# Performance work log

Hardware: AMD Instinct MI355X
Metric: run time of the kernel (lower is better)

## Reference

```python
import jax, jax.numpy as jnp
import numpy as np

B, NUM, NVAR = 2048, 100, 11
NUM_OBS, NC = 10, 3
T_FIN = 10.0
RHO_OBS = 1.0; RHO_INEQ = 1.0; RHO_LANE = 1.0; RHO_PROJ = 1.0
W_SMOOTH = 20.0; W_VDES = 2.0; W_YDES = 1.0
A_EGO = 3.0; B_EGO = 1.5; MARGIN = 0.2
V_MIN = 0.001; V_MAX = 18.0; A_MAX = 6.0
MAXITER = 5
H = 256

def _basis():
    s = np.linspace(0.0, 1.0, NUM)
    j = np.arange(NVAR)
    P = s[:, None] ** j[None, :]
    Pd = np.zeros((NUM, NVAR)); Pdd = np.zeros((NUM, NVAR))
    Pd[:, 1:] = j[1:][None, :] * s[:, None] ** (j[1:] - 1)[None, :]
    Pdd[:, 2:] = (j[2:] * (j[2:] - 1))[None, :] * s[:, None] ** (j[2:] - 2)[None, :]
    return (jnp.asarray(P, jnp.float32), jnp.asarray(Pd / T_FIN, jnp.float32),
            jnp.asarray(Pdd / (T_FIN ** 2), jnp.float32))

P, PDOT, PDDOT = _basis()
A_EQ_X = jnp.stack([P[0], PDOT[0], PDDOT[0], P[-1]])   # [4, NVAR]
A_EQ_Y = jnp.stack([P[0], PDOT[0], PDDOT[0]])          # [3, NVAR]
PTP = P.T @ P

def _kkt_inv(Q, A):
    m = A.shape[0]
    K = jnp.concatenate([jnp.concatenate([Q, A.T], axis=1),
                         jnp.concatenate([A, jnp.zeros((m, m), jnp.float32)], axis=1)], axis=0)
    return jnp.linalg.inv(K)

# ADMM cost: rho_proj*I + smoothness + rho_obs*A_obs^T A_obs + rho_ineq*(Pdot^T Pdot + Pddot^T Pddot)
Q_COMMON = (RHO_PROJ + W_SMOOTH) * jnp.eye(NVAR, dtype=jnp.float32) \
    + RHO_OBS * NUM_OBS * NC * PTP \
    + RHO_INEQ * (PDOT.T @ PDOT + PDDOT.T @ PDDOT)
KKT_X = _kkt_inv(Q_COMMON, A_EQ_X)
KKT_Y = _kkt_inv(Q_COMMON + 2.0 * RHO_LANE * PTP, A_EQ_Y)   # A_lane = [P; -P]
# x_init QP (smoothness + v_des / y_des tracking)
Q_IX = W_SMOOTH * jnp.eye(NVAR, dtype=jnp.float32) + W_VDES * (PDOT.T @ PDOT)
KKT_IX = _kkt_inv(Q_IX, A_EQ_X)
KKT_IY = _kkt_inv(Q_IX + W_YDES * PTP, A_EQ_Y)


def _forward(init_state_ego, goal_des, closest_obs, psi_obs, dim_x_obs, dim_y_obs,
             y_ub, y_lb, gru_W_ih, gru_W_hh, gru_b, gru_h0,
             mlp_W1, mlp_b1, mlp_W2, mlp_b2):
    b = init_state_ego.shape[0]
    x0, y0, vx0, vy0, ax0, ay0 = (init_state_ego[:, i] for i in range(6))
    b_eq_x = jnp.stack([x0, vx0, ax0, goal_des[:, 0]], axis=1)   # [B,4]
    b_eq_y = jnp.stack([y0, vy0, ay0], axis=1)                    # [B,3]

    # ---- obstacle circle trajectories (static obstacles, vx=vy=0) ----
    xo = closest_obs[:, :NUM_OBS]; yo = closest_obs[:, NUM_OBS:2 * NUM_OBS]   # [B,O]
    r = jnp.stack([jnp.zeros_like(dim_x_obs),
                   (dim_x_obs - dim_y_obs) / 2,
                   -(dim_x_obs - dim_y_obs) / 2], axis=2)                      # [B,O,3]
    x_circ = xo[:, :, None] + r * jnp.cos(psi_obs)[:, :, None]                # [B,O,3]
    y_circ = yo[:, :, None] + r * jnp.sin(psi_obs)[:, :, None]
    shape4 = (b, NUM_OBS, NC, NUM)
    x_obs_f = jnp.broadcast_to(x_circ[..., None], shape4).reshape(b, -1)      # [B,O*C*T]
    y_obs_f = jnp.broadcast_to(y_circ[..., None], shape4).reshape(b, -1)
    rad = dim_y_obs / 2
    a_obs = jnp.broadcast_to((A_EGO + rad + MARGIN)[:, :, None, None], shape4).reshape(b, -1)
    b_obs = jnp.broadcast_to((B_EGO + rad + MARGIN)[:, :, None, None], shape4).reshape(b, -1)

    # ---- GRU context over obstacles -> learned lambda init ----
    feats = jnp.stack([xo, yo, dim_x_obs, dim_y_obs, psi_obs], axis=2)        # [B,O,5]
    def gru_step(h, x):
        gx = x @ gru_W_ih + gru_b
        gh = h @ gru_W_hh
        z = jax.nn.sigmoid(gx[:, :H] + gh[:, :H])
        rg = jax.nn.sigmoid(gx[:, H:2 * H] + gh[:, H:2 * H])
        n = jnp.tanh(gx[:, 2 * H:] + rg * gh[:, 2 * H:])
        return (1.0 - z) * n + z * h, None
    hT, _ = jax.lax.scan(gru_step, jnp.broadcast_to(gru_h0, (b, H)), jnp.swapaxes(feats, 0, 1))
    lam = jax.nn.relu(hT @ mlp_W1 + mlp_b1) @ mlp_W2 + mlp_b2                 # [B,2*NVAR]
    lam_x, lam_y = lam[:, :NVAR], lam[:, NVAR:]

    # ---- x_init: equality-constrained smoothness/tracking QP ----
    v_des = jnp.sqrt(vx0 ** 2 + vy0 ** 2)
    lin_ix = W_VDES * v_des[:, None] * jnp.sum(PDOT, axis=0)[None, :]
    lin_iy = W_YDES * goal_des[:, 1:2] * jnp.sum(P, axis=0)[None, :]
    c_x0 = (jnp.concatenate([lin_ix, b_eq_x], 1) @ KKT_IX.T)[:, :NVAR]
    c_y0 = (jnp.concatenate([lin_iy, b_eq_y], 1) @ KKT_IY.T)[:, :NVAR]

    b_lane = jnp.concatenate([y_ub[:, None] * jnp.ones((1, NUM), jnp.float32),
                              -y_lb[:, None] * jnp.ones((1, NUM), jnp.float32)], axis=1)  # [B,2T]

    def AobsT(v):   # A_obs^T v, v: [B, O*C*T] -> [B, NVAR]
        return v.reshape(b, NUM_OBS * NC, NUM).sum(axis=1) @ P

    def step(carry, _):
        c_x, c_y, lx, ly = carry
        x = c_x @ P.T; xd = c_x @ PDOT.T; xdd = c_x @ PDDOT.T
        y = c_y @ P.T; yd = c_y @ PDOT.T; ydd = c_y @ PDDOT.T
        wc = jnp.tile(x, (1, NUM_OBS * NC)) - x_obs_f
        ws = jnp.tile(y, (1, NUM_OBS * NC)) - y_obs_f
        alpha_o = jnp.arctan2(ws * a_obs, wc * b_obs)
        ca, sa = jnp.cos(alpha_o), jnp.sin(alpha_o)
        c1 = RHO_OBS * (a_obs ** 2 * ca ** 2 + b_obs ** 2 * sa ** 2)
        c2 = RHO_OBS * (a_obs * wc * ca + b_obs * ws * sa)
        d_o = jnp.maximum(1.0, c2 / c1)
        alpha_v = jnp.clip(jnp.arctan2(yd, xd), -0.41, 0.41)
        cv, sv = jnp.cos(alpha_v), jnp.sin(alpha_v)
        d_v = jnp.clip(xd * cv + yd * sv, V_MIN, V_MAX)
        alpha_a = jnp.arctan2(ydd + 1e-4, xdd + 1e-4)
        caa, saa = jnp.cos(alpha_a), jnp.sin(alpha_a)
        d_a = jnp.clip(xdd * caa + ydd * saa, 0.0, A_MAX)
        # targets
        b_ox = x_obs_f + a_obs * d_o * ca; b_oy = y_obs_f + b_obs * d_o * sa
        b_vx = d_v * cv; b_vy = d_v * sv
        b_ax = d_a * caa; b_ay = d_a * saa
        b_lane_aug = jnp.minimum(jnp.concatenate([y, -y], 1), b_lane)  # slack-augmented
        top_x = lx + RHO_PROJ * c_x0 + RHO_OBS * AobsT(b_ox) + RHO_INEQ * (b_vx @ PDOT + b_ax @ PDDOT)
        top_y = ly + RHO_PROJ * c_y0 + RHO_OBS * AobsT(b_oy) + RHO_INEQ * (b_vy @ PDOT + b_ay @ PDDOT) \
            + RHO_LANE * ((b_lane_aug[:, :NUM] - b_lane_aug[:, NUM:]) @ P)
        c_xn = (jnp.concatenate([top_x, b_eq_x], 1) @ KKT_X.T)[:, :NVAR]
        c_yn = (jnp.concatenate([top_y, b_eq_y], 1) @ KKT_Y.T)[:, :NVAR]
        # residuals / Lagrange multiplier updates
        xn = c_xn @ P.T; yn = c_yn @ P.T
        res_ox = jnp.tile(xn, (1, NUM_OBS * NC)) - b_ox
        res_oy = jnp.tile(yn, (1, NUM_OBS * NC)) - b_oy
        lxn = lx - RHO_OBS * AobsT(res_ox) \
            - RHO_INEQ * ((c_xn @ PDOT.T - b_vx) @ PDOT + (c_xn @ PDDOT.T - b_ax) @ PDDOT)
        res_lane = jnp.concatenate([yn, -yn], 1) - b_lane_aug
        lyn = ly - RHO_OBS * AobsT(res_oy) \
            - RHO_INEQ * ((c_yn @ PDOT.T - b_vy) @ PDOT + (c_yn @ PDDOT.T - b_ay) @ PDDOT) \
            - RHO_LANE * ((res_lane[:, :NUM] - res_lane[:, NUM:]) @ P)
        return (c_xn, c_yn, lxn, lyn), None

    (c_x, c_y, lam_x, lam_y), _ = jax.lax.scan(step, (c_x0, c_y0, lam_x, lam_y),
                                               None, length=MAXITER)
    return jnp.concatenate([c_x, c_y], axis=1)   # [B, 2*NVAR]


def setup_inputs() -> dict:
    key = jax.random.key(0)
    ks = jax.random.split(key, 12)
    d = {
        'init_state_ego': jax.random.normal(ks[0], (B, 6), jnp.float32),
        'goal_des': jax.random.normal(ks[1], (B, 2), jnp.float32),
        'closest_obs': jax.random.normal(ks[2], (B, 2 * NUM_OBS), jnp.float32),
        'psi_obs': jax.random.normal(ks[3], (B, NUM_OBS), jnp.float32),
        'dim_x_obs': jax.random.uniform(ks[4], (B, NUM_OBS), jnp.float32),
        'dim_y_obs': jax.random.uniform(ks[5], (B, NUM_OBS), jnp.float32),
        'y_ub': jnp.ones((B,), jnp.float32),
        'y_lb': jnp.zeros((B,), jnp.float32),
        'gru_W_ih': jax.random.normal(ks[6], (5, 3 * H), jnp.float32) / np.sqrt(5.0),
        'gru_W_hh': jax.random.normal(ks[7], (H, 3 * H), jnp.float32) / np.sqrt(float(H)),
        'gru_b': jnp.zeros((3 * H,), jnp.float32),
        'gru_h0': jax.random.normal(ks[8], (H,), jnp.float32) * 0.1,
        'mlp_W1': jax.random.normal(ks[9], (H, 512), jnp.float32) / np.sqrt(float(H)),
        'mlp_b1': jnp.zeros((512,), jnp.float32),
        'mlp_W2': jax.random.normal(ks[10], (512, 2 * NVAR), jnp.float32) / np.sqrt(512.0),
        'mlp_b2': jnp.zeros((2 * NVAR,), jnp.float32),
    }
    return d


def reference(init_state_ego, goal_des, closest_obs, psi_obs, dim_x_obs, dim_y_obs,
              y_ub, y_lb, gru_W_ih, gru_W_hh, gru_b, gru_h0,
              mlp_W1, mlp_b1, mlp_W2, mlp_b2):
    return _forward(init_state_ego, goal_des, closest_obs, psi_obs, dim_x_obs, dim_y_obs,
                    y_ub, y_lb, gru_W_ih, gru_W_hh, gru_b, gru_h0,
                    mlp_W1, mlp_b1, mlp_W2, mlp_b2)
```

## Files before the change

### kernel.cpp

```cpp
#include <hip/hip_runtime.h>
#include <math.h>

typedef short bf16x8 __attribute__((ext_vector_type(8)));
typedef float f32x4 __attribute__((ext_vector_type(4)));

__device__ __forceinline__ unsigned short f2bf(float x) {
  union { float f; unsigned u; } v; v.f = x;
  unsigned r = v.u + 0x7FFFu + ((v.u >> 16) & 1u);
  return (unsigned short)(r >> 16);
}
__device__ __forceinline__ float bf2f(unsigned short h) {
  union { unsigned u; float f; } v; v.u = ((unsigned)h) << 16; return v.f;
}

#define WS_WAUG  0u
#define WS_W1T   442368u
#define WS_HAUGA 704512u
#define WS_HAUGB 1884160u
#define WS_HF32  3063808u
#define WS_LAM   5160960u
#define WS_KKT   5341184u
#define WS_GX    5344000u
#define WS_GY    5344704u
#define WS_MX    5345408u
#define WS_MY    5346112u
#define WS_SUMS  5346816u
#define WS_W2T   5346944u

__global__ __launch_bounds__(256) void prep(
    const float* __restrict__ Whh, const float* __restrict__ Wih,
    const float* __restrict__ gb, const float* __restrict__ W1,
    const float* __restrict__ W2, const float* __restrict__ h0,
    const float* __restrict__ obs, const float* __restrict__ dimx,
    const float* __restrict__ dimy, const float* __restrict__ psi,
    unsigned short* __restrict__ Waug, unsigned short* __restrict__ W1T,
    unsigned short* __restrict__ W2T,
    unsigned short* __restrict__ HaugA, unsigned short* __restrict__ HaugB,
    float* __restrict__ kkt_out, float* __restrict__ Gx_out,
    float* __restrict__ Gy_out, float* __restrict__ Mx_out,
    float* __restrict__ My_out, float* __restrict__ sums_out)
{
  __shared__ double S[21];
  __shared__ double aug[15][32];
  __shared__ double fbuf[15];
  __shared__ double Md[11][11];
  if (blockIdx.x < 4) {
    const int mat = blockIdx.x;
    const int n = (mat == 0 || mat == 2) ? 15 : 14;
    const int twoN = 2 * n;
    if (threadIdx.x == 0) {
      for (int m = 0; m < 21; ++m) S[m] = 0.0;
      for (int s = 0; s < 100; ++s) {
        double t = s * (1.0 / 99.0);
        double p = 1.0;
        for (int m = 0; m < 21; ++m) { S[m] += p; p *= t; }
      }
    }
    __syncthreads();
    for (int idx = threadIdx.x; idx < n * twoN; idx += 256) {
      int r = idx / twoN, c = idx % twoN;
      double v;
      if (c >= n) v = (c - n == r) ? 1.0 : 0.0;
      else if (r < 11 && c < 11) {
        double ptp = S[r + c];
        double pdp = (r >= 1 && c >= 1) ? ((double)(r * c) / 100.0) * S[r + c - 2] : 0.0;
        double pddp = (r >= 2 && c >= 2) ? ((double)(r*(r-1)) * (double)(c*(c-1)) / 10000.0) * S[r + c - 4] : 0.0;
        double dg = (r == c) ? 1.0 : 0.0;
        if (mat == 0)      v = 21.0*dg + 30.0*ptp + pdp + pddp;
        else if (mat == 1) v = 21.0*dg + 32.0*ptp + pdp + pddp;
        else if (mat == 2) v = 20.0*dg + 2.0*pdp;
        else               v = 20.0*dg + 2.0*pdp + ptp;
      } else if (r >= 11 && c >= 11) v = 0.0;
      else {
        int ar = (r >= 11) ? (r - 11) : (c - 11);
        int ac = (r >= 11) ? c : r;
        v = (ar == 0) ? ((ac == 0) ? 1.0 : 0.0)
          : (ar == 1) ? ((ac == 1) ? 0.1 : 0.0)
          : (ar == 2) ? ((ac == 2) ? 0.02 : 0.0)
          : 1.0;
      }
      aug[r][c] = v;
    }
    __syncthreads();
    for (int p = 0; p < n; ++p) {
      double pv = aug[p][p];
      __syncthreads();
      double inv = 1.0 / pv;
      for (int c = threadIdx.x; c < twoN; c += 256) aug[p][c] *= inv;
      __syncthreads();
      if (threadIdx.x < n) fbuf[threadIdx.x] = aug[threadIdx.x][p];
      __syncthreads();
      for (int idx = threadIdx.x; idx < n * twoN; idx += 256) {
        int r = idx / twoN, c = idx % twoN;
        if (r != p) aug[r][c] -= fbuf[r] * aug[p][c];
      }
      __syncthreads();
    }
    for (int idx = threadIdx.x; idx < 11 * n; idx += 256) {
      int r = idx / n, c = idx % n;
      kkt_out[mat * 176 + r * 16 + c] = (float)aug[r][n + c];
    }
    if (mat < 2) {
      if (threadIdx.x < 121) {
        int j = threadIdx.x / 11, i = threadIdx.x % 11;
        double m = 30.0 * S[j + i];
        if (j >= 1 && i >= 1) m += ((double)(j * i) / 100.0) * S[j + i - 2];
        if (j >= 2 && i >= 2) m += ((double)(j*(j-1)) * (double)(i*(i-1)) / 10000.0) * S[j + i - 4];
        if (mat == 1) m += 2.0 * S[j + i];
        Md[j][i] = m;
      }
      __syncthreads();
      if (threadIdx.x < 121) {
        int j = threadIdx.x / 11, i = threadIdx.x % 11;
        double g = (j == i) ? 1.0 : 0.0;
        for (int k = 0; k < 11; ++k) g -= Md[j][k] * aug[k][n + i];
        if (mat == 0) { Gx_out[j * 16 + i] = (float)g; Mx_out[j * 16 + i] = (float)Md[j][i]; }
        else          { Gy_out[j * 16 + i] = (float)g; My_out[j * 16 + i] = (float)Md[j][i]; }
      }
    }
    if (mat == 0 && threadIdx.x < 11) {
      int j = threadIdx.x;
      sums_out[j] = (float)S[j];
      sums_out[11 + j] = (j >= 1) ? (float)((double)j / 10.0 * S[j - 1]) : 0.f;
    }
    return;
  }
  int idx = (blockIdx.x - 4) * 256 + threadIdx.x;
  if (idx < 221184) {
    int col = idx / 288, k = idx - col * 288;
    float v;
    if (k < 256)       v = Whh[k * 768 + col];
    else if (k < 261)  v = Wih[(k - 256) * 768 + col];
    else if (k == 261) v = gb[col];
    else               v = 0.f;
    Waug[idx] = f2bf(v);
  } else if (idx < 352256) {
    int j = idx - 221184;
    int col = j >> 8, k = j & 255;
    W1T[j] = f2bf(W1[k * 512 + col]);
  } else if (idx < 942080) {
    int j = idx - 352256;
    int row = j / 288, k = j - row * 288;
    float v;
    if (k < 256)       v = h0[k];
    else if (k == 256) v = obs[row * 20 + 0];
    else if (k == 257) v = obs[row * 20 + 10];
    else if (k == 258) v = dimx[row * 10 + 0];
    else if (k == 259) v = dimy[row * 10 + 0];
    else if (k == 260) v = psi[row * 10 + 0];
    else if (k == 261) v = 1.0f;
    else               v = 0.f;
    HaugA[row * 288 + k] = f2bf(v);
  } else if (idx < 995328) {
    int j = idx - 942080;
    int row = j / 26, k = 262 + (j - row * 26);
    HaugB[row * 288 + k] = 0;
  } else if (idx < 1011712) {
    int j = idx - 995328;
    int col = j >> 9, k = j & 511;
    W2T[j] = f2bf(col < 22 ? W2[k * 22 + col] : 0.f);
  }
}

#define MFMA __builtin_amdgcn_mfma_f32_16x16x32_bf16
__global__ __launch_bounds__(256) void gru_step(
    const unsigned short* __restrict__ Waug,
    const unsigned short* __restrict__ HaugC, unsigned short* __restrict__ HaugN,
    float* __restrict__ Hf32, const float* __restrict__ h0,
    const float* __restrict__ obs, const float* __restrict__ dimx,
    const float* __restrict__ dimy, const float* __restrict__ psi,
    int s)
{
  const int tid = threadIdx.x;
  const int m0 = blockIdx.x * 32;
  const int c0 = blockIdx.y * 32;
  const int lane = tid & 63, w = tid >> 6;
  const int l15 = lane & 15, g4 = lane >> 4;
  const int mi = w >> 1, cg = w & 1;

  const unsigned short* Arow = HaugC + (size_t)(m0 + mi * 16 + l15) * 288 + g4 * 8;
  const unsigned short* Bcol = Waug + (size_t)(c0 + cg * 16 + l15) * 288 + g4 * 8;

  f32x4 accz = {0.f,0.f,0.f,0.f}, accr = {0.f,0.f,0.f,0.f};
  f32x4 anh = {0.f,0.f,0.f,0.f}, anx = {0.f,0.f,0.f,0.f};

  #pragma unroll
  for (int kc = 0; kc < 9; ++kc) {
    bf16x8 a  = *(const bf16x8*)(Arow + kc * 32);
    bf16x8 bz = *(const bf16x8*)(Bcol + kc * 32);
    bf16x8 br = *(const bf16x8*)(Bcol + 256 * 288 + kc * 32);
    bf16x8 bn = *(const bf16x8*)(Bcol + 512 * 288 + kc * 32);
    accz = MFMA(a, bz, accz, 0, 0, 0);
    accr = MFMA(a, br, accr, 0, 0, 0);
    if (kc < 8) anh = MFMA(a, bn, anh, 0, 0, 0);
    else        anx = MFMA(a, bn, anx, 0, 0, 0);
  }

  const int colh = c0 + cg * 16 + l15;
  float h0c = (s == 0) ? h0[colh] : 0.f;
  #pragma unroll
  for (int rg = 0; rg < 4; ++rg) {
    int row = m0 + mi * 16 + g4 * 4 + rg;
    float hold = (s == 0) ? h0c : Hf32[(size_t)row * 256 + colh];
    float z = 1.f / (1.f + __expf(-accz[rg]));
    float rr = 1.f / (1.f + __expf(-accr[rg]));
    float nn = tanhf(anx[rg] + rr * anh[rg]);
    float hnew = (1.f - z) * nn + z * hold;
    Hf32[(size_t)row * 256 + colh] = hnew;
    HaugN[(size_t)row * 288 + colh] = f2bf(hnew);
  }
  if (blockIdx.y == 0 && s < 9 && tid < 192) {
    int row = m0 + tid / 6, e = tid - (tid / 6) * 6;
    int s1 = s + 1;
    float v = (e == 0) ? obs[row * 20 + s1] : (e == 1) ? obs[row * 20 + 10 + s1]
            : (e == 2) ? dimx[row * 10 + s1] : (e == 3) ? dimy[row * 10 + s1]
            : (e == 4) ? psi[row * 10 + s1] : 1.0f;
    HaugN[(size_t)row * 288 + 256 + e] = f2bf(v);
  }
}

__global__ __launch_bounds__(256) void mlp_fused(
    const unsigned short* __restrict__ Haug, const unsigned short* __restrict__ W1T,
    const float* __restrict__ b1, const unsigned short* __restrict__ W2T,
    const float* __restrict__ b2, float* __restrict__ lam)
{
  __shared__ __align__(16) unsigned short As[4096];
  __shared__ __align__(16) unsigned short Acts[8192];
  const int tid = threadIdx.x;
  const int m0 = blockIdx.x * 16;
  const int lane = tid & 63, w = tid >> 6, l15 = lane & 15, g4 = lane >> 4;

  #pragma unroll
  for (int r = 0; r < 2; ++r) {
    int j = tid + 256 * r;
    int tile = j >> 6, q = j & 63, ci = q >> 2, ks = q & 3;
    const unsigned short* src = Haug + (size_t)(m0 + ci) * 288 + tile * 32 + ks * 8;
    *(int4*)&As[tile * 512 + q * 8] = *(const int4*)src;
  }
  __syncthreads();
  const int foff = (l15 * 4 + g4) * 8;

  f32x4 acc[8];
  #pragma unroll
  for (int nt = 0; nt < 8; ++nt) acc[nt] = (f32x4){0.f,0.f,0.f,0.f};
  #pragma unroll
  for (int kc = 0; kc < 8; ++kc) {
    bf16x8 a = *(const bf16x8*)&As[kc * 512 + foff];
    int kk = kc * 32 + g4 * 8;
    #pragma unroll
    for (int nt = 0; nt < 8; ++nt) {
      int col = w * 128 + nt * 16 + l15;
      bf16x8 b = *(const bf16x8*)&W1T[(size_t)col * 256 + kk];
      acc[nt] = MFMA(a, b, acc[nt], 0, 0, 0);
    }
  }
  #pragma unroll
  for (int nt = 0; nt < 8; ++nt) {
    int col = w * 128 + nt * 16 + l15;
    float bb = b1[col];
    int tile = col >> 5, sub = (col >> 3) & 3, e = col & 7;
    #pragma unroll
    for (int rg = 0; rg < 4; ++rg) {
      int row = g4 * 4 + rg;
      float v = fmaxf(acc[nt][rg] + bb, 0.f);
      Acts[tile * 512 + (row * 4 + sub) * 8 + e] = f2bf(v);
    }
  }
  __syncthreads();

  if (w < 2) {
    int col = w * 16 + l15;
    f32x4 a2 = {0.f,0.f,0.f,0.f};
    #pragma unroll
    for (int kc = 0; kc < 16; ++kc) {
      bf16x8 a = *(const bf16x8*)&Acts[kc * 512 + foff];
      bf16x8 b = *(const bf16x8*)&W2T[(size_t)col * 512 + kc * 32 + g4 * 8];
      a2 = MFMA(a, b, a2, 0, 0, 0);
    }
    if (col < 22) {
      float bb = b2[col];
      #pragma unroll
      for (int rg = 0; rg < 4; ++rg)
        lam[(size_t)(m0 + g4 * 4 + rg) * 22 + col] = a2[rg] + bb;
    }
  }
}

__global__ __launch_bounds__(128) void solver(
    const float* __restrict__ ise, const float* __restrict__ goal,
    const float* __restrict__ obs, const float* __restrict__ psi,
    const float* __restrict__ dimx, const float* __restrict__ dimy,
    const float* __restrict__ yub, const float* __restrict__ ylb,
    const float* __restrict__ lam, const float* __restrict__ kkt,
    const float* __restrict__ Gxm, const float* __restrict__ Gym,
    const float* __restrict__ Mxm, const float* __restrict__ Mym,
    const float* __restrict__ sums, float* __restrict__ out)
{
  __shared__ __align__(16) float Pt[3][11][108];
  __shared__ __align__(16) float red[7][108];
  __shared__ float redout[7][11];
  __shared__ float cx[11], cy[11], lx[11], ly[11], cx0[11], cy0[11];
  __shared__ float kxB[11], kyB[11], hx[11], hy[11];
  __shared__ float rhsx[15], rhsy[14];
  __shared__ float xc[30], yc[30], sa_[10], sb_[10], sab[10], sab2[10];

  const int b = blockIdx.x;
  const int tid = threadIdx.x;

  if (tid < 100) {
    float t = tid * (1.0f / 99.0f);
    float tjm2 = 0.f, tjm1 = 0.f, tj = 1.f;
    #pragma unroll
    for (int j = 0; j < 11; ++j) {
      Pt[0][j][tid] = tj;
      Pt[1][j][tid] = 0.1f * (float)j * tjm1;
      Pt[2][j][tid] = 0.01f * (float)(j * (j - 1)) * tjm2;
      tjm2 = tjm1; tjm1 = tj; tj *= t;
    }
  }
  if (tid < 10) {
    int o = tid;
    float xo = obs[b * 20 + o], yo = obs[b * 20 + 10 + o];
    float dx = dimx[b * 10 + o], dy = dimy[b * 10 + o], ps = psi[b * 10 + o];
    float sp, cp;
    __sincosf(ps, &sp, &cp);
    float r1 = 0.5f * (dx - dy);
    xc[o * 3] = xo; xc[o * 3 + 1] = xo + r1 * cp; xc[o * 3 + 2] = xo - r1 * cp;
    yc[o * 3] = yo; yc[o * 3 + 1] = yo + r1 * sp; yc[o * 3 + 2] = yo - r1 * sp;
    float rad = 0.5f * dy;
    float av = 3.2f + rad, bv = 1.7f + rad;
    sa_[o] = av; sb_[o] = bv; sab[o] = av * bv; sab2[o] = av * bv * av * bv;
  }
  if (tid < 11) { lx[tid] = lam[b * 22 + tid]; ly[tid] = lam[b * 22 + 11 + tid]; }
  const float vx0 = ise[b * 6 + 2], vy0 = ise[b * 6 + 3];
  if (tid == 0) {
    float x0 = ise[b * 6 + 0], y0 = ise[b * 6 + 1];
    float ax0 = ise[b * 6 + 4], ay0 = ise[b * 6 + 5];
    rhsx[11] = x0; rhsx[12] = vx0; rhsx[13] = ax0; rhsx[14] = goal[b * 2 + 0];
    rhsy[11] = y0; rhsy[12] = vy0; rhsy[13] = ay0;
  }
  {
    float vdes = sqrtf(vx0 * vx0 + vy0 * vy0);
    float gy = goal[b * 2 + 1];
    if (tid < 11) { rhsx[tid] = 2.f * vdes * sums[11 + tid]; rhsy[tid] = gy * sums[tid]; }
  }
  const float yU = yub[b], yL = ylb[b];
  __syncthreads();
  if (tid < 11) {
    const float* K = kkt + 2 * 176 + tid * 16;
    float s = 0.f;
    #pragma unroll
    for (int j = 0; j < 15; ++j) s += K[j] * rhsx[j];
    cx0[tid] = s; cx[tid] = s;
    const float* Kx = kkt + tid * 16;
    float kb = 0.f;
    #pragma unroll
    for (int c = 0; c < 4; ++c) kb += Kx[11 + c] * rhsx[11 + c];
    kxB[tid] = kb;
  } else if (tid >= 16 && tid < 27) {
    int i = tid - 16;
    const float* K = kkt + 3 * 176 + i * 16;
    float s = 0.f;
    #pragma unroll
    for (int j = 0; j < 14; ++j) s += K[j] * rhsy[j];
    cy0[i] = s; cy[i] = s;
    const float* Ky = kkt + 176 + i * 16;
    float kb = 0.f;
    #pragma unroll
    for (int c = 0; c < 3; ++c) kb += Ky[11 + c] * rhsy[11 + c];
    kyB[i] = kb;
  }
  __syncthreads();
  if (tid < 11) {
    float s = cx0[tid];
    #pragma unroll
    for (int i = 0; i < 11; ++i) s += Mxm[tid * 16 + i] * kxB[i];
    hx[tid] = s;
  } else if (tid >= 16 && tid < 27) {
    int j = tid - 16;
    float s = cy0[j];
    #pragma unroll
    for (int i = 0; i < 11; ++i) s += Mym[j * 16 + i] * kyB[i];
    hy[j] = s;
  }
  __syncthreads();

  for (int it = 0; it < 5; ++it) {
    if (tid < 100) {
      float t = tid * (1.0f / 99.0f);
      float x = 0, y = 0, xd = 0, yd = 0, xdd = 0, ydd = 0;
      {
        float tjm2 = 0, tjm1 = 0, tj = 1;
        #pragma unroll
        for (int j = 0; j < 11; ++j) {
          float cj = cx[j], dj = cy[j];
          x += cj * tj; y += dj * tj;
          float pd = 0.1f * (float)j * tjm1;
          xd += cj * pd; yd += dj * pd;
          float pdd = 0.01f * (float)(j * (j - 1)) * tjm2;
          xdd += cj * pdd; ydd += dj * pdd;
          tjm2 = tjm1; tjm1 = tj; tj *= t;
        }
      }
      float Sbx = 0.f, Sby = 0.f;
      for (int oi = 0; oi < 10; ++oi) {
        float A = sa_[oi], B = sb_[oi], AB = sab[oi], AB2 = sab2[oi];
        #pragma unroll
        for (int cc = 0; cc < 3; ++cc) {
          int o = oi * 3 + cc;
          float xcc = xc[o], ycc = yc[o];
          float wc = x - xcc, wsv = y - ycc;
          float p = wsv * A, q = wc * B;
          float h2 = p * p + q * q;
          float rin = rsqrtf(h2 + 1e-20f);
          float sc = AB * rin;
          bool outside = h2 >= AB2;
          Sbx += outside ? x : fmaf(wc, sc, xcc);
          Sby += outside ? y : fmaf(wsv, sc, ycc);
        }
      }
      bool clipv = (xd <= 0.f) || (fabsf(yd) > xd * 0.43463135f);
      float cv, sv;
      if (clipv) { cv = 0.91712081f; sv = copysignf(0.39860934f, yd); }
      else { float ri = rsqrtf(fmaxf(xd * xd + yd * yd, 1e-24f)); cv = xd * ri; sv = yd * ri; }
      float dv = fminf(fmaxf(xd * cv + yd * sv, 0.001f), 18.f);
      float qa = xdd + 1e-4f, pa = ydd + 1e-4f;
      float ria = rsqrtf(pa * pa + qa * qa + 1e-30f);
      float caa = qa * ria, saa = pa * ria;
      float da = fminf(fmaxf(xdd * caa + ydd * saa, 0.f), 6.f);
      red[0][tid] = Sbx; red[1][tid] = Sby;
      red[2][tid] = dv * cv; red[3][tid] = dv * sv;
      red[4][tid] = da * caa; red[5][tid] = da * saa;
      red[6][tid] = fminf(y, yU) - fminf(-y, -yL);
    }
    __syncthreads();
    if (tid < 77) {
      int a = tid / 11, j = tid - a * 11;
      int wt = (a < 2) ? 0 : (a < 4) ? 1 : (a < 6) ? 2 : 0;
      const float4* rp = (const float4*)(&red[a][0]);
      const float4* wp = (const float4*)(&Pt[wt][j][0]);
      float s = 0.f;
      #pragma unroll
      for (int k = 0; k < 25; ++k) {
        float4 rv = rp[k], wv = wp[k];
        s += rv.x * wv.x + rv.y * wv.y + rv.z * wv.z + rv.w * wv.w;
      }
      redout[a][j] = s;
    }
    __syncthreads();
    if (tid < 11) {
      const float* K = kkt + tid * 16;
      const float* G = Gxm + tid * 16;
      float sc = kxB[tid], sl = -hx[tid];
      #pragma unroll
      for (int i = 0; i < 11; ++i) {
        float r = lx[i] + cx0[i] + redout[0][i] + redout[2][i] + redout[4][i];
        sc += K[i] * r;
        sl += G[i] * r;
      }
      cx[tid] = sc; lx[tid] = sl;
    } else if (tid >= 16 && tid < 27) {
      int j = tid - 16;
      const float* K = kkt + 176 + j * 16;
      const float* G = Gym + j * 16;
      float sc = kyB[j], sl = -hy[j];
      #pragma unroll
      for (int i = 0; i < 11; ++i) {
        float r = ly[i] + cy0[i] + redout[1][i] + redout[3][i] + redout[5][i] + redout[6][i];
        sc += K[i] * r;
        sl += G[i] * r;
      }
      cy[j] = sc; ly[j] = sl;
    }
    __syncthreads();
  }
  if (tid < 11) out[b * 22 + tid] = cx[tid];
  else if (tid >= 16 && tid < 27) out[b * 22 + 11 + (tid - 16)] = cy[tid - 16];
}

extern "C" void kernel_launch(void* const* d_in, const int* in_sizes, int n_in,
                              void* d_out, int out_size, void* d_ws, size_t ws_size,
                              hipStream_t stream) {
  const float* ise  = (const float*)d_in[0];
  const float* goal = (const float*)d_in[1];
  const float* obs  = (const float*)d_in[2];
  const float* psi  = (const float*)d_in[3];
  const float* dimx = (const float*)d_in[4];
  const float* dimy = (const float*)d_in[5];
  const float* yub  = (const float*)d_in[6];
  const float* ylb  = (const float*)d_in[7];
  const float* Wih  = (const float*)d_in[8];
  const float* Whh  = (const float*)d_in[9];
  const float* gb   = (const float*)d_in[10];
  const float* h0   = (const float*)d_in[11];
  const float* W1   = (const float*)d_in[12];
  const float* b1   = (const float*)d_in[13];
  const float* W2   = (const float*)d_in[14];
  const float* b2   = (const float*)d_in[15];

  char* ws = (char*)d_ws;
  unsigned short* Waug  = (unsigned short*)(ws + WS_WAUG);
  unsigned short* W1T   = (unsigned short*)(ws + WS_W1T);
  unsigned short* W2T   = (unsigned short*)(ws + WS_W2T);
  unsigned short* HaugA = (unsigned short*)(ws + WS_HAUGA);
  unsigned short* HaugB = (unsigned short*)(ws + WS_HAUGB);
  float* Hf32 = (float*)(ws + WS_HF32);
  float* lamb = (float*)(ws + WS_LAM);
  float* kkt  = (float*)(ws + WS_KKT);
  float* Gxm  = (float*)(ws + WS_GX);
  float* Gym  = (float*)(ws + WS_GY);
  float* Mxm  = (float*)(ws + WS_MX);
  float* Mym  = (float*)(ws + WS_MY);
  float* sums = (float*)(ws + WS_SUMS);

  prep<<<3956, 256, 0, stream>>>(Whh, Wih, gb, W1, W2, h0, obs, dimx, dimy, psi,
                                 Waug, W1T, W2T, HaugA, HaugB,
                                 kkt, Gxm, Gym, Mxm, Mym, sums);
  for (int s = 0; s < 10; ++s) {
    const unsigned short* hc = (s & 1) ? HaugB : HaugA;
    unsigned short* hn = (s & 1) ? HaugA : HaugB;
    gru_step<<<dim3(64, 8), 256, 0, stream>>>(Waug, hc, hn, Hf32, h0,
                                              obs, dimx, dimy, psi, s);
  }
  mlp_fused<<<128, 256, 0, stream>>>(HaugA, W1T, b1, W2T, b2, lamb);
  solver<<<2048, 128, 0, stream>>>(ise, goal, obs, psi, dimx, dimy, yub, ylb,
                                   lamb, kkt, Gxm, Gym, Mxm, Mym, sums, (float*)d_out);
  (void)in_sizes; (void)n_in; (void)out_size; (void)ws_size;
}
```

Measured before the change: 262.9 us.

## Pack two batch elements per solver block and precompute ADMM RHS once

The solver kernel now handles two batch elements per 256-thread block, and all per-element shared state is duplicated with a pair index, so the basis table Pt is built once and shared by both. The ADMM right-hand side is also computed into shared memory once per iteration instead of being recomputed inside the 11-term dot product by every output thread. The aim is to amortise the basis setup, halve the block count, and cut redundant shared reads. The cost is one extra barrier per iteration, and every barrier now spans both elements.

```diff
diff --git a/kernel.cpp b/kernel.cpp
--- a/kernel.cpp
+++ b/kernel.cpp
@@ -286,7 +286,7 @@
   }
 }
 
-__global__ __launch_bounds__(128) void solver(
+__global__ __launch_bounds__(256) void solver(
     const float* __restrict__ ise, const float* __restrict__ goal,
     const float* __restrict__ obs, const float* __restrict__ psi,
     const float* __restrict__ dimx, const float* __restrict__ dimy,
@@ -297,15 +297,16 @@
     const float* __restrict__ sums, float* __restrict__ out)
 {
   __shared__ __align__(16) float Pt[3][11][108];
-  __shared__ __align__(16) float red[7][108];
-  __shared__ float redout[7][11];
-  __shared__ float cx[11], cy[11], lx[11], ly[11], cx0[11], cy0[11];
-  __shared__ float kxB[11], kyB[11], hx[11], hy[11];
-  __shared__ float rhsx[15], rhsy[14];
-  __shared__ float xc[30], yc[30], sa_[10], sb_[10], sab[10], sab2[10];
-
-  const int b = blockIdx.x;
+  __shared__ __align__(16) float red[2][7][108];
+  __shared__ float redout[2][7][11];
+  __shared__ float cx[2][11], cy[2][11], lx[2][11], ly[2][11], cx0[2][11], cy0[2][11];
+  __shared__ float kxB[2][11], kyB[2][11], hx[2][11], hy[2][11];
+  __shared__ float rhsx[2][15], rhsy[2][14];
+  __shared__ float xc[2][30], yc[2][30], sa_[2][10], sb_[2][10], sab[2][10], sab2[2][10];
+
   const int tid = threadIdx.x;
+  const int pr = tid >> 7, lt = tid & 127;
+  const int b = blockIdx.x * 2 + pr;
 
   if (tid < 100) {
     float t = tid * (1.0f / 99.0f);
@@ -318,82 +319,82 @@
       tjm2 = tjm1; tjm1 = tj; tj *= t;
     }
   }
-  if (tid < 10) {
-    int o = tid;
+  if (lt < 10) {
+    int o = lt;
     float xo = obs[b * 20 + o], yo = obs[b * 20 + 10 + o];
     float dx = dimx[b * 10 + o], dy = dimy[b * 10 + o], ps = psi[b * 10 + o];
     float sp, cp;
     __sincosf(ps, &sp, &cp);
     float r1 = 0.5f * (dx - dy);
-    xc[o * 3] = xo; xc[o * 3 + 1] = xo + r1 * cp; xc[o * 3 + 2] = xo - r1 * cp;
-    yc[o * 3] = yo; yc[o * 3 + 1] = yo + r1 * sp; yc[o * 3 + 2] = yo - r1 * sp;
+    xc[pr][o * 3] = xo; xc[pr][o * 3 + 1] = xo + r1 * cp; xc[pr][o * 3 + 2] = xo - r1 * cp;
+    yc[pr][o * 3] = yo; yc[pr][o * 3 + 1] = yo + r1 * sp; yc[pr][o * 3 + 2] = yo - r1 * sp;
     float rad = 0.5f * dy;
     float av = 3.2f + rad, bv = 1.7f + rad;
-    sa_[o] = av; sb_[o] = bv; sab[o] = av * bv; sab2[o] = av * bv * av * bv;
-  }
-  if (tid < 11) { lx[tid] = lam[b * 22 + tid]; ly[tid] = lam[b * 22 + 11 + tid]; }
+    sa_[pr][o] = av; sb_[pr][o] = bv; sab[pr][o] = av * bv; sab2[pr][o] = av * bv * av * bv;
+  }
+  if (lt < 11) { lx[pr][lt] = lam[b * 22 + lt]; ly[pr][lt] = lam[b * 22 + 11 + lt]; }
   const float vx0 = ise[b * 6 + 2], vy0 = ise[b * 6 + 3];
-  if (tid == 0) {
+  if (lt == 0) {
     float x0 = ise[b * 6 + 0], y0 = ise[b * 6 + 1];
     float ax0 = ise[b * 6 + 4], ay0 = ise[b * 6 + 5];
-    rhsx[11] = x0; rhsx[12] = vx0; rhsx[13] = ax0; rhsx[14] = goal[b * 2 + 0];
-    rhsy[11] = y0; rhsy[12] = vy0; rhsy[13] = ay0;
+    rhsx[pr][11] = x0; rhsx[pr][12] = vx0; rhsx[pr][13] = ax0; rhsx[pr][14] = goal[b * 2 + 0];
+    rhsy[pr][11] = y0; rhsy[pr][12] = vy0; rhsy[pr][13] = ay0;
   }
   {
     float vdes = sqrtf(vx0 * vx0 + vy0 * vy0);
     float gy = goal[b * 2 + 1];
-    if (tid < 11) { rhsx[tid] = 2.f * vdes * sums[11 + tid]; rhsy[tid] = gy * sums[tid]; }
+    if (lt < 11) { rhsx[pr][lt] = 2.f * vdes * sums[11 + lt]; rhsy[pr][lt] = gy * sums[lt]; }
   }
   const float yU = yub[b], yL = ylb[b];
   __syncthreads();
-  if (tid < 11) {
-    const float* K = kkt + 2 * 176 + tid * 16;
+  if (lt < 11) {
+    const float* K = kkt + 2 * 176 + lt * 16;
     float s = 0.f;
     #pragma unroll
-    for (int j = 0; j < 15; ++j) s += K[j] * rhsx[j];
-    cx0[tid] = s; cx[tid] = s;
-    const float* Kx = kkt + tid * 16;
+    for (int j = 0; j < 15; ++j) s += K[j] * rhsx[pr][j];
+    cx0[pr][lt] = s; cx[pr][lt] = s;
+    const float* Kx = kkt + lt * 16;
     float kb = 0.f;
     #pragma unroll
-    for (int c = 0; c < 4; ++c) kb += Kx[11 + c] * rhsx[11 + c];
-    kxB[tid] = kb;
-  } else if (tid >= 16 && tid < 27) {
-    int i = tid - 16;
+    for (int c = 0; c < 4; ++c) kb += Kx[11 + c] * rhsx[pr][11 + c];
+    kxB[pr][lt] = kb;
+  } else if (lt >= 16 && lt < 27) {
+    int i = lt - 16;
     const float* K = kkt + 3 * 176 + i * 16;
     float s = 0.f;
     #pragma unroll
-    for (int j = 0; j < 14; ++j) s += K[j] * rhsy[j];
-    cy0[i] = s; cy[i] = s;
+    for (int j = 0; j < 14; ++j) s += K[j] * rhsy[pr][j];
+    cy0[pr][i] = s; cy[pr][i] = s;
     const float* Ky = kkt + 176 + i * 16;
     float kb = 0.f;
     #pragma unroll
-    for (int c = 0; c < 3; ++c) kb += Ky[11 + c] * rhsy[11 + c];
-    kyB[i] = kb;
+    for (int c = 0; c < 3; ++c) kb += Ky[11 + c] * rhsy[pr][11 + c];
+    kyB[pr][i] = kb;
   }
   __syncthreads();
-  if (tid < 11) {
-    float s = cx0[tid];
-    #pragma unroll
-    for (int i = 0; i < 11; ++i) s += Mxm[tid * 16 + i] * kxB[i];
-    hx[tid] = s;
-  } else if (tid >= 16 && tid < 27) {
-    int j = tid - 16;
-    float s = cy0[j];
-    #pragma unroll
-    for (int i = 0; i < 11; ++i) s += Mym[j * 16 + i] * kyB[i];
-    hy[j] = s;
+  if (lt < 11) {
+    float s = cx0[pr][lt];
+    #pragma unroll
+    for (int i = 0; i < 11; ++i) s += Mxm[lt * 16 + i] * kxB[pr][i];
+    hx[pr][lt] = s;
+  } else if (lt >= 16 && lt < 27) {
+    int j = lt - 16;
+    float s = cy0[pr][j];
+    #pragma unroll
+    for (int i = 0; i < 11; ++i) s += Mym[j * 16 + i] * kyB[pr][i];
+    hy[pr][j] = s;
   }
   __syncthreads();
 
   for (int it = 0; it < 5; ++it) {
-    if (tid < 100) {
-      float t = tid * (1.0f / 99.0f);
+    if (lt < 100) {
+      float t = lt * (1.0f / 99.0f);
       float x = 0, y = 0, xd = 0, yd = 0, xdd = 0, ydd = 0;
       {
         float tjm2 = 0, tjm1 = 0, tj = 1;
         #pragma unroll
         for (int j = 0; j < 11; ++j) {
-          float cj = cx[j], dj = cy[j];
+          float cj = cx[pr][j], dj = cy[pr][j];
           x += cj * tj; y += dj * tj;
           float pd = 0.1f * (float)j * tjm1;
           xd += cj * pd; yd += dj * pd;
@@ -404,11 +405,11 @@
       }
       float Sbx = 0.f, Sby = 0.f;
       for (int oi = 0; oi < 10; ++oi) {
-        float A = sa_[oi], B = sb_[oi], AB = sab[oi], AB2 = sab2[oi];
+        float A = sa_[pr][oi], B = sb_[pr][oi], AB = sab[pr][oi], AB2 = sab2[pr][oi];
         #pragma unroll
         for (int cc = 0; cc < 3; ++cc) {
           int o = oi * 3 + cc;
-          float xcc = xc[o], ycc = yc[o];
+          float xcc = xc[pr][o], ycc = yc[pr][o];
           float wc = x - xcc, wsv = y - ycc;
           float p = wsv * A, q = wc * B;
           float h2 = p * p + q * q;
@@ -428,16 +429,16 @@
       float ria = rsqrtf(pa * pa + qa * qa + 1e-30f);
       float caa = qa * ria, saa = pa * ria;
       float da = fminf(fmaxf(xdd * caa + ydd * saa, 0.f), 6.f);
-      red[0][tid] = Sbx; red[1][tid] = Sby;
-      red[2][tid] = dv * cv; red[3][tid] = dv * sv;
-      red[4][tid] = da * caa; red[5][tid] = da * saa;
-      red[6][tid] = fminf(y, yU) - fminf(-y, -yL);
+      red[pr][0][lt] = Sbx; red[pr][1][lt] = Sby;
+      red[pr][2][lt] = dv * cv; red[pr][3][lt] = dv * sv;
+      red[pr][4][lt] = da * caa; red[pr][5][lt] = da * saa;
+      red[pr][6][lt] = fminf(y, yU) - fminf(-y, -yL);
     }
     __syncthreads();
-    if (tid < 77) {
-      int a = tid / 11, j = tid - a * 11;
+    if (lt < 77) {
+      int a = lt / 11, j = lt - a * 11;
       int wt = (a < 2) ? 0 : (a < 4) ? 1 : (a < 6) ? 2 : 0;
-      const float4* rp = (const float4*)(&red[a][0]);
+      const float4* rp = (const float4*)(&red[pr][a][0]);
       const float4* wp = (const float4*)(&Pt[wt][j][0]);
       float s = 0.f;
       #pragma unroll
@@ -445,37 +446,44 @@
         float4 rv = rp[k], wv = wp[k];
         s += rv.x * wv.x + rv.y * wv.y + rv.z * wv.z + rv.w * wv.w;
       }
-      redout[a][j] = s;
+      redout[pr][a][j] = s;
     }
     __syncthreads();
-    if (tid < 11) {
-      const float* K = kkt + tid * 16;
-      const float* G = Gxm + tid * 16;
-      float sc = kxB[tid], sl = -hx[tid];
+    if (lt < 11)
+      rhsx[pr][lt] = lx[pr][lt] + cx0[pr][lt] + redout[pr][0][lt] + redout[pr][2][lt] + redout[pr][4][lt];
+    else if (lt >= 16 && lt < 27) {
+      int j = lt - 16;
+      rhsy[pr][j] = ly[pr][j] + cy0[pr][j] + redout[pr][1][j] + redout[pr][3][j] + redout[pr][5][j] + redout[pr][6][j];
+    }
+    __syncthreads();
+    if (lt < 11) {
+      const float* K = kkt + lt * 16;
+      const float* G = Gxm + lt * 16;
+      float sc = kxB[pr][lt], sl = -hx[pr][lt];
       #pragma unroll
       for (int i = 0; i < 11; ++i) {
-        float r = lx[i] + cx0[i] + redout[0][i] + redout[2][i] + redout[4][i];
+        float r = rhsx[pr][i];
         sc += K[i] * r;
         sl += G[i] * r;
       }
-      cx[tid] = sc; lx[tid] = sl;
-    } else if (tid >= 16 && tid < 27) {
-      int j = tid - 16;
+      cx[pr][lt] = sc; lx[pr][lt] = sl;
+    } else if (lt >= 16 && lt < 27) {
+      int j = lt - 16;
       const float* K = kkt + 176 + j * 16;
       const float* G = Gym + j * 16;
-      float sc = kyB[j], sl = -hy[j];
+      float sc = kyB[pr][j], sl = -hy[pr][j];
       #pragma unroll
       for (int i = 0; i < 11; ++i) {
-        float r = ly[i] + cy0[i] + redout[1][i] + redout[3][i] + redout[5][i] + redout[6][i];
+        float r = rhsy[pr][i];
         sc += K[i] * r;
         sl += G[i] * r;
       }
-      cy[j] = sc; ly[j] = sl;
+      cy[pr][j] = sc; ly[pr][j] = sl;
     }
     __syncthreads();
   }
-  if (tid < 11) out[b * 22 + tid] = cx[tid];
-  else if (tid >= 16 && tid < 27) out[b * 22 + 11 + (tid - 16)] = cy[tid - 16];
+  if (lt < 11) out[b * 22 + lt] = cx[pr][lt];
+  else if (lt >= 16 && lt < 27) out[b * 22 + 11 + (lt - 16)] = cy[pr][lt - 16];
 }
 
 extern "C" void kernel_launch(void* const* d_in, const int* in_sizes, int n_in,
@@ -523,7 +531,7 @@
                                               obs, dimx, dimy, psi, s);
   }
   mlp_fused<<<128, 256, 0, stream>>>(HaugA, W1T, b1, W2T, b2, lamb);
-  solver<<<2048, 128, 0, stream>>>(ise, goal, obs, psi, dimx, dimy, yub, ylb,
+  solver<<<1024, 256, 0, stream>>>(ise, goal, obs, psi, dimx, dimy, yub, ylb,
                                    lamb, kkt, Gxm, Gym, Mxm, Mym, sums, (float*)d_out);
   (void)in_sizes; (void)n_in; (void)out_size; (void)ws_size;
 }
```

Result: faster. 241.4 us (-8.2%).
